# Performance work log

Hardware: AMD Instinct MI355X
Metric: run time of the kernel (lower is better)

## Reference

```python
import jax, jax.numpy as jnp
import numpy as np

RES = 32          # resolution (32, 32) -> N = 1024 tokens
HEADS = 16
EMB = 1024
BATCH = 8
N = RES * RES


def _bias_idxs(res):
    # relative-offset index table, [N, N] with values in [0, res*res)
    coords = np.stack(np.meshgrid(np.arange(res), np.arange(res), indexing='ij'), -1).reshape(-1, 2)
    d = np.abs(coords[:, None, :] - coords[None, :, :])  # [N, N, 2]
    return jnp.asarray(d[..., 0] * res + d[..., 1], dtype=jnp.int64)


def setup_inputs() -> dict:
    key = jax.random.key(0)
    k1, k2, k3, k4, k5 = jax.random.split(key, 5)
    x = jax.random.normal(k1, (BATCH, N, EMB), dtype=jnp.float32)
    w_qkv = jax.random.normal(k2, (3 * EMB, EMB), dtype=jnp.float32) * 0.02
    biases = jax.random.normal(k3, (HEADS, RES * RES), dtype=jnp.float32) * 0.02
    bias_idxs = _bias_idxs(RES)
    w_out = jax.random.normal(k4, (EMB, EMB), dtype=jnp.float32) * 0.02
    b_out = jax.random.normal(k5, (EMB,), dtype=jnp.float32) * 0.02
    return {"x": x, "w_qkv": w_qkv, "biases": biases,
            "bias_idxs": bias_idxs, "w_out": w_out, "b_out": b_out}


def reference(x, w_qkv, biases, bias_idxs, w_out, b_out):
    b, n, e = x.shape
    h = HEADS
    d = e // h
    scale = d ** -0.5
    # to_qkv: Linear(e, 3e, bias=False); torch Linear computes x @ W.T
    qkv = x @ w_qkv.T                                   # [b, n, 3e]
    q, k, v = jnp.split(qkv, 3, axis=-1)
    def to_heads(t):
        return t.reshape(b, n, h, d).transpose(0, 2, 1, 3)  # b h n d
    q, k, v = to_heads(q), to_heads(k), to_heads(v)
    scores = jnp.einsum('bhid,bhjd->bhij', q, k) * scale    # [b, h, n, n]
    scores = scores + biases[:, bias_idxs]                  # gather -> [h, n, n], broadcast over b
    attn = jax.nn.softmax(scores, axis=-1)
    out = jnp.einsum('bhij,bhjd->bhid', attn, v)            # [b, h, n, d]
    out = out.transpose(0, 2, 1, 3).reshape(b, n, e)        # b n (h d)
    # to_out: Linear(e, e) with bias (dropout = identity at inference)
    return out @ w_out.T + b_out
```

## Files before the change

### kernel.cpp

```cpp
#include <hip/hip_runtime.h>
#include <stdint.h>


#define LOG2E 1.4426950408889634f

typedef __attribute__((ext_vector_type(8))) short short8;
typedef __attribute__((ext_vector_type(4))) short short4v;
typedef __attribute__((ext_vector_type(4))) float floatx4;
typedef __attribute__((ext_vector_type(2))) unsigned int uint2v;

__device__ __forceinline__ short f2bf(float f) {
  uint32_t u = __builtin_bit_cast(uint32_t, f);
  u = (u + 0x7FFFu + ((u >> 16) & 1u)) >> 16;
  return (short)(uint16_t)u;
}
__device__ __forceinline__ float bf2f(short s) {
  uint32_t u = ((uint32_t)(uint16_t)s) << 16;
  return __builtin_bit_cast(float, u);
}
__device__ __forceinline__ float fast_exp2(float x) {
#if __has_builtin(__builtin_amdgcn_exp2f)
  return __builtin_amdgcn_exp2f(x);
#else
  return exp2f(x);
#endif
}

__device__ __forceinline__ void gload_lds16(const short* g, short* l) {
  __builtin_amdgcn_global_load_lds(
      (const __attribute__((address_space(1))) void*)g,
      (__attribute__((address_space(3))) void*)l, 16, 0, 0);
}

__global__ void cvt_bf16(const float* __restrict__ src, short* __restrict__ dst, int n4) {
  int i = blockIdx.x * 256 + threadIdx.x;
  if (i >= n4) return;
  float4 f = ((const float4*)src)[i];
  short4v o;
  o.x = f2bf(f.x); o.y = f2bf(f.y); o.z = f2bf(f.z); o.w = f2bf(f.w);
  ((short4v*)dst)[i] = o;
}

__global__ void bias_precomp(const float* __restrict__ biases, short* __restrict__ biast) {
  int t = blockIdx.x * 256 + threadIdx.x;
  int lane = t & 63;
  int tile = t >> 6;
  int jt = tile & 63, it = (tile >> 6) & 63, h = tile >> 12;
  int i0 = it * 16 + ((lane >> 4) << 2);
  int j = jt * 16 + (lane & 15);
  int rj = j >> 5, cj = j & 31;
  short4v o;
#pragma unroll
  for (int r = 0; r < 4; r++) {
    int i = i0 + r;
    int ri = i >> 5, ci = i & 31;
    int dr = ri - rj; if (dr < 0) dr = -dr;
    int dc = ci - cj; if (dc < 0) dc = -dc;
    o[r] = f2bf(biases[h * 1024 + dr * 32 + dc] * LOG2E);
  }
  *(short4v*)&biast[(size_t)t * 4] = o;
}

template <int MODE>
__global__ __launch_bounds__(256, 2) void gemm_bt(
    const short* __restrict__ A, const short* __restrict__ Bt,
    short* __restrict__ qo, short* __restrict__ ko, short* __restrict__ vto,
    const float* __restrict__ bvec, float* __restrict__ outf) {
  __shared__ __align__(16) short sA[128 * 64];
  __shared__ __align__(16) short sB[128 * 64];
  const int tid = threadIdx.x;
  const int w = tid >> 6, lane = tid & 63;
  const int wr = w >> 1, wc = w & 1;
  const int bm = blockIdx.y, bn = blockIdx.x;
  const int qd = lane >> 4, col = lane & 15;

  floatx4 acc[4][4] = {};
  const int rowA0 = bm * 128, rowB0 = bn * 128;
  const int ciw = w * 256;

  for (int kk = 0; kk < 1024; kk += 64) {
    __syncthreads();
#pragma unroll
    for (int n = 0; n < 4; n++) {
      int ci = ciw + n * 64 + lane;
      int r = ci >> 3, c = (ci & 7) ^ (r & 7);
      gload_lds16(A + (size_t)(rowA0 + r) * 1024 + kk + c * 8, &sA[ci * 8]);
    }
#pragma unroll
    for (int n = 0; n < 4; n++) {
      int ci = ciw + n * 64 + lane;
      int r = ci >> 3, c = (ci & 7) ^ (r & 7);
      gload_lds16(Bt + (size_t)(rowB0 + r) * 1024 + kk + c * 8, &sB[ci * 8]);
    }
    __syncthreads();

#pragma unroll
    for (int ks = 0; ks < 2; ks++) {
      const int ch = qd + ks * 4;
      short8 af[4], bff[4];
#pragma unroll
      for (int rt = 0; rt < 4; rt++) {
        int r = wr * 64 + rt * 16 + col;
        af[rt] = *(const short8*)&sA[r * 64 + ((ch ^ (r & 7)) << 3)];
      }
#pragma unroll
      for (int ct = 0; ct < 4; ct++) {
        int r = wc * 64 + ct * 16 + col;
        bff[ct] = *(const short8*)&sB[r * 64 + ((ch ^ (r & 7)) << 3)];
      }
#pragma unroll
      for (int rt = 0; rt < 4; rt++)
#pragma unroll
        for (int ct = 0; ct < 4; ct++)
          acc[rt][ct] = __builtin_amdgcn_mfma_f32_16x16x32_bf16(af[rt], bff[ct], acc[rt][ct], 0, 0, 0);
    }
  }

  if (MODE == 0) {
    if (bn >= 16) {
#pragma unroll
      for (int rt = 0; rt < 4; rt++) {
#pragma unroll
        for (int ct = 0; ct < 4; ct++) {
          int Cg = bn * 128 + wc * 64 + ct * 16 + col;
          int e = Cg & 1023, h = e >> 6, dd = e & 63;
          short4v pv;
#pragma unroll
          for (int r = 0; r < 4; r++) pv[r] = f2bf(acc[rt][ct][r]);
          int R0 = bm * 128 + wr * 64 + rt * 16 + qd * 4;
          int b = R0 >> 10, n0 = R0 & 1023;
          int bh = b * 16 + h;
          *(short4v*)&vto[((size_t)bh * 64 + dd) * 1024 + n0] = pv;
        }
      }
    } else {
#pragma unroll
      for (int rt = 0; rt < 4; rt++) {
#pragma unroll
        for (int ct = 0; ct < 4; ct++) {
          int Cg = bn * 128 + wc * 64 + ct * 16 + col;
          int which = Cg >> 10, e = Cg & 1023, h = e >> 6, dd = e & 63;
#pragma unroll
          for (int r = 0; r < 4; r++) {
            int R = bm * 128 + wr * 64 + rt * 16 + qd * 4 + r;
            int b = R >> 10, n = R & 1023;
            int bh = b * 16 + h;
            short v = f2bf(acc[rt][ct][r]);
            if (which == 0)
              qo[((size_t)bh * 1024 + n) * 64 + dd] = v;
            else
              ko[((size_t)bh * 1024 + n) * 64 + dd] = v;
          }
        }
      }
    }
  } else {
#pragma unroll
    for (int rt = 0; rt < 4; rt++)
#pragma unroll
      for (int ct = 0; ct < 4; ct++) {
        int Cg = bn * 128 + wc * 64 + ct * 16 + col;
        float bo = bvec[Cg];
#pragma unroll
        for (int r = 0; r < 4; r++) {
          int R = bm * 128 + wr * 64 + rt * 16 + qd * 4 + r;
          outf[(size_t)R * 1024 + Cg] = acc[rt][ct][r] + bo;
        }
      }
  }
}

__global__ __launch_bounds__(256, 2) void attn_fused(
    const short* __restrict__ q, const short* __restrict__ k,
    const short* __restrict__ vt, const short* __restrict__ biast,
    short* __restrict__ ao) {
  __shared__ __align__(16) short sK[128 * 64];
  __shared__ __align__(16) short sVt[64 * 128];
  __shared__ __align__(16) short sP[128 * 136];
  const int tid = threadIdx.x, w = tid >> 6, lane = tid & 63;
  const int bh = blockIdx.x, qt = blockIdx.y;
  const int h = bh & 15;
  const int qd = lane >> 4, col = lane & 15;
  const short* qb = q + (size_t)bh * 65536;
  const short* kb = k + (size_t)bh * 65536;
  const short* vb = vt + (size_t)bh * 65536;
  const int ciw = w * 256;

#pragma unroll
  for (int n = 0; n < 4; n++) {
    int ci = ciw + n * 64 + lane;
    int r = ci >> 3, c = (ci & 7) ^ (r & 7);
    gload_lds16(qb + (size_t)(qt * 128 + r) * 64 + c * 8, &sP[ci * 8]);
  }
  __syncthreads();
  short8 bq[2][8];
#pragma unroll
  for (int ks = 0; ks < 2; ks++) {
    const int ch = qd + ks * 4;
#pragma unroll
    for (int ct = 0; ct < 8; ct++) {
      int r2 = ct * 16 + col;
      bq[ks][ct] = *(const short8*)&sP[r2 * 64 + ((ch ^ (r2 & 7)) << 3)];
    }
  }

  floatx4 oacc[2][4] = {};
  float lsum[8] = {0, 0, 0, 0, 0, 0, 0, 0};
  const float SCL = 0.125f * LOG2E;

  for (int js = 0; js < 8; js++) {
    __syncthreads();
#pragma unroll
    for (int n = 0; n < 4; n++) {
      int ci = ciw + n * 64 + lane;
      int r = ci >> 3, c = (ci & 7) ^ (r & 7);
      gload_lds16(kb + (size_t)(js * 128 + r) * 64 + c * 8, &sK[ci * 8]);
    }
#pragma unroll
    for (int n = 0; n < 4; n++) {
      int ci = ciw + n * 64 + lane;
      int r = ci >> 4, c = (ci & 15) ^ (r & 15);
      gload_lds16(vb + (size_t)r * 1024 + js * 128 + c * 8, &sVt[ci * 8]);
    }
    __syncthreads();

    short4v bfrag[2][8];
#pragma unroll
    for (int rt = 0; rt < 2; rt++) {
      int a = js * 8 + w * 2 + rt;
#pragma unroll
      for (int ct = 0; ct < 8; ct++) {
        int b = qt * 8 + ct;
        bfrag[rt][ct] = *(const short4v*)&biast[((((size_t)h * 64 + a) * 64 + b) << 8) + lane * 4];
      }
    }

#pragma unroll
    for (int rt = 0; rt < 2; rt++) {
      floatx4 sacc[8] = {};
#pragma unroll
      for (int ks = 0; ks < 2; ks++) {
        const int ch = qd + ks * 4;
        int r = w * 32 + rt * 16 + col;
        short8 ak = *(const short8*)&sK[r * 64 + ((ch ^ (r & 7)) << 3)];
#pragma unroll
        for (int ct = 0; ct < 8; ct++)
          sacc[ct] = __builtin_amdgcn_mfma_f32_16x16x32_bf16(ak, bq[ks][ct], sacc[ct], 0, 0, 0);
      }
      const int s = w * 8 + rt * 4 + qd;
#pragma unroll
      for (int ct = 0; ct < 8; ct++) {
        int i = ct * 16 + col;
        float e0 = fast_exp2(fmaf(sacc[ct][0], SCL, bf2f(bfrag[rt][ct][0])));
        float e1 = fast_exp2(fmaf(sacc[ct][1], SCL, bf2f(bfrag[rt][ct][1])));
        float e2 = fast_exp2(fmaf(sacc[ct][2], SCL, bf2f(bfrag[rt][ct][2])));
        float e3 = fast_exp2(fmaf(sacc[ct][3], SCL, bf2f(bfrag[rt][ct][3])));
        lsum[ct] += (e0 + e1) + (e2 + e3);
        uint32_t u0 = __builtin_bit_cast(uint32_t, e0) + 0x8000u;
        uint32_t u1 = __builtin_bit_cast(uint32_t, e1) + 0x8000u;
        uint32_t u2 = __builtin_bit_cast(uint32_t, e2) + 0x8000u;
        uint32_t u3 = __builtin_bit_cast(uint32_t, e3) + 0x8000u;
        uint2v pk;
        pk.x = __builtin_amdgcn_perm(u1, u0, 0x07060302u);
        pk.y = __builtin_amdgcn_perm(u3, u2, 0x07060302u);
        *(uint2v*)&sP[i * 136 + s * 4] = pk;
      }
    }
    __syncthreads();

#pragma unroll
    for (int ks = 0; ks < 4; ks++) {
      const int ch = ks * 4 + qd;
      short8 ap[2], bv[4];
#pragma unroll
      for (int rt = 0; rt < 2; rt++) {
        int m = w * 32 + rt * 16 + col;
        ap[rt] = *(const short8*)&sP[m * 136 + ch * 8];
      }
#pragma unroll
      for (int ct = 0; ct < 4; ct++) {
        int d = ct * 16 + col;
        bv[ct] = *(const short8*)&sVt[d * 128 + ((ch ^ (d & 15)) << 3)];
      }
#pragma unroll
      for (int rt = 0; rt < 2; rt++)
#pragma unroll
        for (int ct = 0; ct < 4; ct++)
          oacc[rt][ct] = __builtin_amdgcn_mfma_f32_16x16x32_bf16(ap[rt], bv[ct], oacc[rt][ct], 0, 0, 0);
    }
  }

#pragma unroll
  for (int ct = 0; ct < 8; ct++) {
    float v = lsum[ct];
    v += __shfl_xor(v, 16);
    v += __shfl_xor(v, 32);
    lsum[ct] = v;
  }
  float* red = (float*)sK;
  if (lane < 16) {
#pragma unroll
    for (int ct = 0; ct < 8; ct++) red[w * 128 + ct * 16 + lane] = lsum[ct];
  }
  __syncthreads();

  float inv[2][4];
#pragma unroll
  for (int rt = 0; rt < 2; rt++)
#pragma unroll
    for (int r = 0; r < 4; r++) {
      int i = w * 32 + rt * 16 + qd * 4 + r;
      float t = (red[i] + red[128 + i]) + (red[256 + i] + red[384 + i]);
      inv[rt][r] = 1.0f / t;
    }

  const int b = bh >> 4;
#pragma unroll
  for (int rt = 0; rt < 2; rt++)
#pragma unroll
    for (int ct = 0; ct < 4; ct++)
#pragma unroll
      for (int r = 0; r < 4; r++) {
        int n = qt * 128 + w * 32 + rt * 16 + qd * 4 + r;
        int dd = ct * 16 + col;
        ao[(((size_t)b * 1024 + n) << 10) + h * 64 + dd] = f2bf(oacc[rt][ct][r] * inv[rt][r]);
      }
}

extern "C" void kernel_launch(void* const* d_in, const int* in_sizes, int n_in,
                              void* d_out, int out_size, void* d_ws, size_t ws_size,
                              hipStream_t stream) {
  const float* x = (const float*)d_in[0];
  const float* w_qkv = (const float*)d_in[1];
  const float* biases = (const float*)d_in[2];
  const float* w_out = (const float*)d_in[4];
  const float* b_out = (const float*)d_in[5];
  float* out = (float*)d_out;

  char* ws = (char*)d_ws;
  short* xb    = (short*)(ws + 0);
  short* wqkvb = (short*)(ws + 16777216);
  short* woutb = (short*)(ws + 23068672);
  short* qb    = (short*)(ws + 25165824);
  short* kb    = (short*)(ws + 41943040);
  short* vtb   = (short*)(ws + 58720256);
  short* aob   = (short*)(ws + 75497472);
  short* biast = (short*)(ws + 92274688);

  cvt_bf16<<<8192, 256, 0, stream>>>(x, xb, 8192 * 1024 / 4);
  cvt_bf16<<<3072, 256, 0, stream>>>(w_qkv, wqkvb, 3072 * 1024 / 4);
  cvt_bf16<<<1024, 256, 0, stream>>>(w_out, woutb, 1024 * 1024 / 4);
  bias_precomp<<<16384, 256, 0, stream>>>(biases, biast);

  gemm_bt<0><<<dim3(24, 64), 256, 0, stream>>>(xb, wqkvb, qb, kb, vtb, nullptr, nullptr);
  attn_fused<<<dim3(128, 8), 256, 0, stream>>>(qb, kb, vtb, biast, aob);
  gemm_bt<1><<<dim3(8, 64), 256, 0, stream>>>(aob, woutb, nullptr, nullptr, nullptr, b_out, out);
}
```

Measured before the change: 272.0 us.

## Alias K and P LDS buffers, compute row sums via MFMA, raise occupancy

The attention kernel now shares one LDS buffer between the K tile and the probability tile. K fragments are pulled into registers before an extra barrier so P can overwrite that buffer, and P uses an XOR-swizzled layout in place of padding. Softmax row sums are accumulated by an extra MFMA against a vector of bf16 ones, which removes the shuffle-and-LDS reduction at the end. Bias loads and score MFMAs are split into half-width groups to lower register pressure, and launch bounds ask for three blocks per CU. The trade-off is an extra barrier per iteration, extra MFMAs for the sums, and denominators built from bf16-rounded probabilities.

```diff
diff --git a/kernel.cpp b/kernel.cpp
--- a/kernel.cpp
+++ b/kernel.cpp
@@ -170,13 +170,12 @@
   }
 }
 
-__global__ __launch_bounds__(256, 2) void attn_fused(
+__global__ __launch_bounds__(256, 3) void attn_fused(
     const short* __restrict__ q, const short* __restrict__ k,
     const short* __restrict__ vt, const short* __restrict__ biast,
     short* __restrict__ ao) {
-  __shared__ __align__(16) short sK[128 * 64];
+  __shared__ __align__(16) short sPK[128 * 128];
   __shared__ __align__(16) short sVt[64 * 128];
-  __shared__ __align__(16) short sP[128 * 136];
   const int tid = threadIdx.x, w = tid >> 6, lane = tid & 63;
   const int bh = blockIdx.x, qt = blockIdx.y;
   const int h = bh & 15;
@@ -190,7 +189,7 @@
   for (int n = 0; n < 4; n++) {
     int ci = ciw + n * 64 + lane;
     int r = ci >> 3, c = (ci & 7) ^ (r & 7);
-    gload_lds16(qb + (size_t)(qt * 128 + r) * 64 + c * 8, &sP[ci * 8]);
+    gload_lds16(qb + (size_t)(qt * 128 + r) * 64 + c * 8, &sPK[ci * 8]);
   }
   __syncthreads();
   short8 bq[2][8];
@@ -200,12 +199,16 @@
 #pragma unroll
     for (int ct = 0; ct < 8; ct++) {
       int r2 = ct * 16 + col;
-      bq[ks][ct] = *(const short8*)&sP[r2 * 64 + ((ch ^ (r2 & 7)) << 3)];
-    }
-  }
+      bq[ks][ct] = *(const short8*)&sPK[r2 * 64 + ((ch ^ (r2 & 7)) << 3)];
+    }
+  }
+
+  short8 onesf;
+#pragma unroll
+  for (int t = 0; t < 8; t++) onesf[t] = (short)0x3F80;
 
   floatx4 oacc[2][4] = {};
-  float lsum[8] = {0, 0, 0, 0, 0, 0, 0, 0};
+  floatx4 osum[2] = {};
   const float SCL = 0.125f * LOG2E;
 
   for (int js = 0; js < 8; js++) {
@@ -214,7 +217,7 @@
     for (int n = 0; n < 4; n++) {
       int ci = ciw + n * 64 + lane;
       int r = ci >> 3, c = (ci & 7) ^ (r & 7);
-      gload_lds16(kb + (size_t)(js * 128 + r) * 64 + c * 8, &sK[ci * 8]);
+      gload_lds16(kb + (size_t)(js * 128 + r) * 64 + c * 8, &sPK[ci * 8]);
     }
 #pragma unroll
     for (int n = 0; n < 4; n++) {
@@ -224,46 +227,52 @@
     }
     __syncthreads();
 
-    short4v bfrag[2][8];
-#pragma unroll
-    for (int rt = 0; rt < 2; rt++) {
-      int a = js * 8 + w * 2 + rt;
-#pragma unroll
-      for (int ct = 0; ct < 8; ct++) {
-        int b = qt * 8 + ct;
-        bfrag[rt][ct] = *(const short4v*)&biast[((((size_t)h * 64 + a) * 64 + b) << 8) + lane * 4];
-      }
-    }
-
-#pragma unroll
-    for (int rt = 0; rt < 2; rt++) {
-      floatx4 sacc[8] = {};
+    short8 ak[2][2];
+#pragma unroll
+    for (int rt = 0; rt < 2; rt++)
 #pragma unroll
       for (int ks = 0; ks < 2; ks++) {
         const int ch = qd + ks * 4;
         int r = w * 32 + rt * 16 + col;
-        short8 ak = *(const short8*)&sK[r * 64 + ((ch ^ (r & 7)) << 3)];
-#pragma unroll
-        for (int ct = 0; ct < 8; ct++)
-          sacc[ct] = __builtin_amdgcn_mfma_f32_16x16x32_bf16(ak, bq[ks][ct], sacc[ct], 0, 0, 0);
-      }
+        ak[rt][ks] = *(const short8*)&sPK[r * 64 + ((ch ^ (r & 7)) << 3)];
+      }
+    __syncthreads();
+
+#pragma unroll
+    for (int rt = 0; rt < 2; rt++) {
+      const int a = js * 8 + w * 2 + rt;
       const int s = w * 8 + rt * 4 + qd;
 #pragma unroll
-      for (int ct = 0; ct < 8; ct++) {
-        int i = ct * 16 + col;
-        float e0 = fast_exp2(fmaf(sacc[ct][0], SCL, bf2f(bfrag[rt][ct][0])));
-        float e1 = fast_exp2(fmaf(sacc[ct][1], SCL, bf2f(bfrag[rt][ct][1])));
-        float e2 = fast_exp2(fmaf(sacc[ct][2], SCL, bf2f(bfrag[rt][ct][2])));
-        float e3 = fast_exp2(fmaf(sacc[ct][3], SCL, bf2f(bfrag[rt][ct][3])));
-        lsum[ct] += (e0 + e1) + (e2 + e3);
-        uint32_t u0 = __builtin_bit_cast(uint32_t, e0) + 0x8000u;
-        uint32_t u1 = __builtin_bit_cast(uint32_t, e1) + 0x8000u;
-        uint32_t u2 = __builtin_bit_cast(uint32_t, e2) + 0x8000u;
-        uint32_t u3 = __builtin_bit_cast(uint32_t, e3) + 0x8000u;
-        uint2v pk;
-        pk.x = __builtin_amdgcn_perm(u1, u0, 0x07060302u);
-        pk.y = __builtin_amdgcn_perm(u3, u2, 0x07060302u);
-        *(uint2v*)&sP[i * 136 + s * 4] = pk;
+      for (int cg = 0; cg < 2; cg++) {
+        short4v bfrag[4];
+#pragma unroll
+        for (int c4 = 0; c4 < 4; c4++) {
+          int b = qt * 8 + cg * 4 + c4;
+          bfrag[c4] = *(const short4v*)&biast[((((size_t)h * 64 + a) * 64 + b) << 8) + lane * 4];
+        }
+        floatx4 sacc[4] = {};
+#pragma unroll
+        for (int ks = 0; ks < 2; ks++)
+#pragma unroll
+          for (int c4 = 0; c4 < 4; c4++)
+            sacc[c4] = __builtin_amdgcn_mfma_f32_16x16x32_bf16(
+                ak[rt][ks], bq[ks][cg * 4 + c4], sacc[c4], 0, 0, 0);
+#pragma unroll
+        for (int c4 = 0; c4 < 4; c4++) {
+          int i = (cg * 4 + c4) * 16 + col;
+          float e0 = fast_exp2(fmaf(sacc[c4][0], SCL, bf2f(bfrag[c4][0])));
+          float e1 = fast_exp2(fmaf(sacc[c4][1], SCL, bf2f(bfrag[c4][1])));
+          float e2 = fast_exp2(fmaf(sacc[c4][2], SCL, bf2f(bfrag[c4][2])));
+          float e3 = fast_exp2(fmaf(sacc[c4][3], SCL, bf2f(bfrag[c4][3])));
+          uint32_t u0 = __builtin_bit_cast(uint32_t, e0) + 0x8000u;
+          uint32_t u1 = __builtin_bit_cast(uint32_t, e1) + 0x8000u;
+          uint32_t u2 = __builtin_bit_cast(uint32_t, e2) + 0x8000u;
+          uint32_t u3 = __builtin_bit_cast(uint32_t, e3) + 0x8000u;
+          uint2v pk;
+          pk.x = __builtin_amdgcn_perm(u1, u0, 0x07060302u);
+          pk.y = __builtin_amdgcn_perm(u3, u2, 0x07060302u);
+          *(uint2v*)&sPK[i * 128 + ((s ^ (i & 15)) << 2)] = pk;
+        }
       }
     }
     __syncthreads();
@@ -275,7 +284,10 @@
 #pragma unroll
       for (int rt = 0; rt < 2; rt++) {
         int m = w * 32 + rt * 16 + col;
-        ap[rt] = *(const short8*)&sP[m * 136 + ch * 8];
+        int m15 = m & 15;
+        short4v lo = *(const short4v*)&sPK[m * 128 + (((2 * ch) ^ m15) << 2)];
+        short4v hi = *(const short4v*)&sPK[m * 128 + (((2 * ch + 1) ^ m15) << 2)];
+        ap[rt] = __builtin_shufflevector(lo, hi, 0, 1, 2, 3, 4, 5, 6, 7);
       }
 #pragma unroll
       for (int ct = 0; ct < 4; ct++) {
@@ -283,48 +295,30 @@
         bv[ct] = *(const short8*)&sVt[d * 128 + ((ch ^ (d & 15)) << 3)];
       }
 #pragma unroll
-      for (int rt = 0; rt < 2; rt++)
+      for (int rt = 0; rt < 2; rt++) {
 #pragma unroll
         for (int ct = 0; ct < 4; ct++)
           oacc[rt][ct] = __builtin_amdgcn_mfma_f32_16x16x32_bf16(ap[rt], bv[ct], oacc[rt][ct], 0, 0, 0);
-    }
-  }
-
-#pragma unroll
-  for (int ct = 0; ct < 8; ct++) {
-    float v = lsum[ct];
-    v += __shfl_xor(v, 16);
-    v += __shfl_xor(v, 32);
-    lsum[ct] = v;
-  }
-  float* red = (float*)sK;
-  if (lane < 16) {
-#pragma unroll
-    for (int ct = 0; ct < 8; ct++) red[w * 128 + ct * 16 + lane] = lsum[ct];
-  }
-  __syncthreads();
-
-  float inv[2][4];
-#pragma unroll
-  for (int rt = 0; rt < 2; rt++)
-#pragma unroll
-    for (int r = 0; r < 4; r++) {
-      int i = w * 32 + rt * 16 + qd * 4 + r;
-      float t = (red[i] + red[128 + i]) + (red[256 + i] + red[384 + i]);
-      inv[rt][r] = 1.0f / t;
-    }
+        osum[rt] = __builtin_amdgcn_mfma_f32_16x16x32_bf16(ap[rt], onesf, osum[rt], 0, 0, 0);
+      }
+    }
+  }
 
   const int b = bh >> 4;
 #pragma unroll
-  for (int rt = 0; rt < 2; rt++)
+  for (int rt = 0; rt < 2; rt++) {
+    floatx4 inv;
+#pragma unroll
+    for (int r = 0; r < 4; r++) inv[r] = 1.0f / osum[rt][r];
 #pragma unroll
     for (int ct = 0; ct < 4; ct++)
 #pragma unroll
       for (int r = 0; r < 4; r++) {
         int n = qt * 128 + w * 32 + rt * 16 + qd * 4 + r;
         int dd = ct * 16 + col;
-        ao[(((size_t)b * 1024 + n) << 10) + h * 64 + dd] = f2bf(oacc[rt][ct][r] * inv[rt][r]);
-      }
+        ao[(((size_t)b * 1024 + n) << 10) + h * 64 + dd] = f2bf(oacc[rt][ct][r] * inv[r]);
+      }
+  }
 }
 
 extern "C" void kernel_launch(void* const* d_in, const int* in_sizes, int n_in,
```

Result: slower. 332.9 us (+22.4%).
